# Kernel tuning notes

Measured on AMD Instinct MI355X. Metric: run time of the kernel, lower is better.

Reference implementation:

```python
import jax, jax.numpy as jnp
import numpy as np

T = 0.07          # temperature
K_POS = 5         # top-k positives per noun and for mask prediction
MARGIN = 0.1
LAM_CONTRAST = 0.6
LAM_MASK = 0.4


def _l2n(x):
    return x / jnp.linalg.norm(x, axis=-1, keepdims=True)


def setup_inputs() -> dict:
    key = jax.random.key(0)
    k0, k1, k2, k3 = jax.random.split(key, 4)
    B, N, D, M = 64, 576, 512, 16  # N = 24*24 patch grid
    patch_feats = _l2n(jax.random.normal(k0, (B, N, D), jnp.float32))
    noun_feats = _l2n(jax.random.normal(k1, (B, M, D), jnp.float32))
    global_img_feat = _l2n(jax.random.normal(k2, (B, D), jnp.float32))
    global_txt_feat = _l2n(jax.random.normal(k3, (B, D), jnp.float32))
    logit_scale = jnp.full((1,), 1.0 / 0.07, jnp.float32)
    idx = jnp.arange(B, dtype=jnp.int32)
    return {
        "patch_feats": patch_feats,
        "noun_feats": noun_feats,
        "global_img_feat": global_img_feat,
        "global_txt_feat": global_txt_feat,
        "logit_scale": logit_scale,
        "idx": idx,
    }


def _fine_grained_loss(patch_feats, noun_feats):
    # sim[b,m,n] = <noun_m, patch_n>; replaces the nested Python loops.
    B = patch_feats.shape[0]
    sim = jnp.einsum('bmd,bnd->bmn', noun_feats, patch_feats)
    scaled = sim / T
    # Per-noun contrastive loss. log_softmax over cat([topk, rest]) equals
    # log_softmax over all N entries evaluated at the topk positions, so:
    #   loss = -sum_topk log_softmax = K_POS*lse - sum(topk scaled values)
    lse = jax.nn.logsumexp(scaled, axis=-1)              # [B, M]
    topv, _ = jax.lax.top_k(scaled, K_POS)               # [B, M, K]
    contrast_loss = jnp.mean(K_POS * lse - topv.sum(-1))
    # Mask-prediction BCE loss (pool_type='mean').
    pooled = sim.mean(axis=1)                            # [B, N]
    _, tidx = jax.lax.top_k(pooled, K_POS)               # [B, K]
    pred = jnp.zeros_like(pooled).at[jnp.arange(B)[:, None], tidx].set(1.0)
    x = pooled / T
    mask_loss = jnp.mean(jnp.logaddexp(0.0, x) - x * pred)
    return LAM_CONTRAST * contrast_loss + LAM_MASK * mask_loss


def _contrastive_loss(img, txt, logit_scale, idx):
    logits = logit_scale.reshape(()) * (img @ txt.T)
    pos = (idx[:, None] == idx[None, :]).astype(logits.dtype)
    labels = pos / pos.sum(axis=1, keepdims=True)
    li2t = -(jax.nn.log_softmax(logits, axis=1) * labels).sum(1).mean()
    lt2i = -(jax.nn.log_softmax(logits.T, axis=1) * labels).sum(1).mean()
    return 0.5 * (li2t + lt2i)


def _triplet_loss(img, txt):
    scores = img @ txt.T
    d = jnp.diagonal(scores)
    eye = jnp.eye(scores.shape[0], dtype=bool)
    cost_s = jnp.where(eye, 0.0, jnp.clip(MARGIN + scores - d[:, None], 0.0)).sum()
    cost_im = jnp.where(eye, 0.0, jnp.clip(MARGIN + scores - d[None, :], 0.0)).sum()
    return 0.5 * (cost_s + cost_im)


def reference(patch_feats, noun_feats, global_img_feat, global_txt_feat, logit_scale, idx):
    loss_c = _contrastive_loss(global_img_feat, global_txt_feat, logit_scale, idx)
    loss_t = _triplet_loss(global_img_feat, global_txt_feat)
    loss_f = _fine_grained_loss(patch_feats, noun_feats)
    return jnp.stack([loss_c, loss_t, loss_f])
```

## Files before the change

kernel.cpp:

```cpp
#include <hip/hip_runtime.h>
#include <hip/hip_bf16.h>
#include <math.h>

#define NB 64
#define NN 576
#define ND 512
#define NM 16
#define QPB 9
#define KPOS 5
#define TINV 14.2857142857142857f

#define NFINE (NB * QPB)
#define NBLK1 (NFINE + NB)
#define WS_REC_OFF 4096
#define RECSZ 144
#define WS_NOUNF (WS_REC_OFF + NFINE * RECSZ)

#define FINF __builtin_inff()

typedef __attribute__((ext_vector_type(8))) short short8;
typedef __attribute__((ext_vector_type(4))) float floatx4;

__device__ __forceinline__ unsigned pk2(float lo, float hi) {
  return __builtin_amdgcn_perm(__float_as_uint(hi), __float_as_uint(lo), 0x07060302u);
}

__device__ __forceinline__ short8 packB(const float4 a, const float4 b) {
  union { unsigned u[4]; short8 s; } cv;
  cv.u[0] = pk2(a.x, a.y);
  cv.u[1] = pk2(a.z, a.w);
  cv.u[2] = pk2(b.x, b.y);
  cv.u[3] = pk2(b.z, b.w);
  return cv.s;
}

__device__ __forceinline__ void ins5(float (&a)[5], float v) {
  if (v > a[4]) {
    a[4] = v;
    if (a[4] > a[3]) { float x = a[4]; a[4] = a[3]; a[3] = x; }
    if (a[3] > a[2]) { float x = a[3]; a[3] = a[2]; a[2] = x; }
    if (a[2] > a[1]) { float x = a[2]; a[2] = a[1]; a[1] = x; }
    if (a[1] > a[0]) { float x = a[1]; a[1] = a[0]; a[0] = x; }
  }
}

__device__ __forceinline__ void merge5(float (&a)[5], const float (&b)[5]) {
  float r[5];
#pragma unroll
  for (int k = 0; k < 5; ++k) {
    float best = -FINF;
#pragma unroll
    for (int i = 0; i <= k + 1; ++i) {
      const int j = k + 1 - i;
      const float av = (i == 0) ? FINF : a[i - 1];
      const float bv = (j == 0) ? FINF : b[j - 1];
      best = fmaxf(best, fminf(av, bv));
    }
    r[k] = best;
  }
#pragma unroll
  for (int k = 0; k < 5; ++k) a[k] = r[k];
}

__device__ __forceinline__ void merge5_shfl(float (&a)[5], int msk) {
  float o[5];
#pragma unroll
  for (int k = 0; k < 5; ++k) o[k] = __shfl_xor(a[k], msk, 64);
  merge5(a, o);
}

__global__ __launch_bounds__(256) void k_prep(
    const float* __restrict__ noun, float* __restrict__ ws) {
  const int i = blockIdx.x * 256 + threadIdx.x;
  const float4 v = ((const float4*)noun)[i];
  unsigned ux = __float_as_uint(v.x), uy = __float_as_uint(v.y);
  unsigned uz = __float_as_uint(v.z), uw = __float_as_uint(v.w);
  ux += 0x7FFFu + ((ux >> 16) & 1u);
  uy += 0x7FFFu + ((uy >> 16) & 1u);
  uz += 0x7FFFu + ((uz >> 16) & 1u);
  uw += 0x7FFFu + ((uw >> 16) & 1u);
  uint2 o;
  o.x = __builtin_amdgcn_perm(uy, ux, 0x07060302u);
  o.y = __builtin_amdgcn_perm(uw, uz, 0x07060302u);
  ((uint2*)((unsigned short*)(ws + WS_NOUNF)))[i] = o;
}

__global__ __launch_bounds__(256) void k_sim(
    const float* __restrict__ patch, const float* __restrict__ gimg,
    const float* __restrict__ gtxt, float* __restrict__ ws) {
  const int blk = blockIdx.x;
  const int t = threadIdx.x;
  const int lane = t & 63;

  __shared__ float S[NM * 65];

  if (blk < NFINE) {
    const int b = blk / QPB, quad = blk - b * QPB;
    const int w = t >> 6;
    const int nidx = lane & 15;
    const int k0 = (lane >> 4) * 8;

    const unsigned short* nrow =
        (const unsigned short*)(ws + WS_NOUNF) + ((size_t)b * NM + nidx) * ND + k0;
    const float* prow =
        patch + ((size_t)(b * NN + quad * 64 + w * 16 + nidx)) * ND + k0;

    floatx4 acc = {0.f, 0.f, 0.f, 0.f};
#pragma unroll 4
    for (int ks = 0; ks < 16; ++ks) {
      const int o = ks * 32;
      const short8 af = *(const short8*)(nrow + o);
      const float4 p0 = *(const float4*)(prow + o);
      const float4 p1 = *(const float4*)(prow + o + 4);
      const short8 bf = packB(p0, p1);
      acc = __builtin_amdgcn_mfma_f32_16x16x32_bf16(af, bf, acc, 0, 0, 0);
    }

    const int mrow = (lane >> 4) * 4;
    const int pcol = w * 16 + nidx;
#pragma unroll
    for (int r = 0; r < 4; ++r) S[(mrow + r) * 65 + pcol] = acc[r] * TINV;
    __syncthreads();

    float* rec = ws + WS_REC_OFF + (size_t)blk * RECSZ;
    if (w == 1) {
      float x = 0.f;
#pragma unroll
      for (int m = 0; m < NM; ++m) x += S[m * 65 + lane];
      x *= (1.f / 16.f);
      float sxp = (x > 0.f) ? (x + log1pf(expf(-x))) : log1pf(expf(x));
      float t5[5] = {x, -FINF, -FINF, -FINF, -FINF};
#pragma unroll
      for (int msk = 1; msk < 64; msk <<= 1) {
        sxp += __shfl_xor(sxp, msk, 64);
        merge5_shfl(t5, msk);
      }
      if (lane == 0) {
        rec[128] = sxp;
#pragma unroll
        for (int k = 0; k < 5; ++k) rec[129 + k] = t5[k];
      }
    } else if (w == 0) {
      const int r_ = lane & 15;
      const int h = lane >> 4;
      const float* row = &S[r_ * 65 + h * 16];
      float mx = -FINF;
#pragma unroll
      for (int k = 0; k < 16; ++k) mx = fmaxf(mx, row[k]);
      mx = fmaxf(mx, __shfl_xor(mx, 16, 64));
      mx = fmaxf(mx, __shfl_xor(mx, 32, 64));
      float se = 0.f;
      float r5[5] = {-FINF, -FINF, -FINF, -FINF, -FINF};
#pragma unroll
      for (int k = 0; k < 16; ++k) {
        const float v = row[k];
        se += expf(v - mx);
        ins5(r5, v);
      }
      se += __shfl_xor(se, 16, 64);
      se += __shfl_xor(se, 32, 64);
      merge5_shfl(r5, 16);
      merge5_shfl(r5, 32);
      if (h == 0) {
        float* rr = rec + r_ * 8;
        rr[0] = mx;
        rr[1] = se;
#pragma unroll
        for (int k = 0; k < 5; ++k) rr[2 + k] = r5[k];
      }
    }
  } else {
    const int i = blk - NFINE;
    const int dq = t >> 6;
    const float4* ip = (const float4*)(gimg + (size_t)i * ND + dq * 128);
    const float4* tp = (const float4*)(gtxt + (size_t)lane * ND + dq * 128);
    float a = 0.f;
#pragma unroll
    for (int q = 0; q < 32; ++q) {
      const float4 x = ip[q];
      const float4 y = tp[q];
      a += x.x * y.x + x.y * y.y + x.z * y.z + x.w * y.w;
    }
    S[dq * 64 + lane] = a;
    __syncthreads();
    if (t < 64) ws[i * 64 + t] = S[t] + S[64 + t] + S[128 + t] + S[192 + t];
  }
}

__global__ __launch_bounds__(64) void k_final(
    const float* __restrict__ ws, const float* __restrict__ lscale,
    const int* __restrict__ idx, float* __restrict__ out) {
  const int blk = blockIdx.x;
  const int t = threadIdx.x;

  if (blk < NB) {
    const float* base = ws + WS_REC_OFF + (size_t)blk * QPB * RECSZ;
    const int m = t & 15;
    const int g = t >> 4;
    const int nq = (g == 0) ? 3 : 2;

    float lm[3], ls[3];
    float t5[5] = {-FINF, -FINF, -FINF, -FINF, -FINF};
#pragma unroll
    for (int i = 0; i < 3; ++i) { lm[i] = -FINF; ls[i] = 0.f; }
    float mx = -FINF;
    for (int i = 0; i < nq; ++i) {
      const float* rr = base + (g + 4 * i) * RECSZ + m * 8;
      lm[i] = rr[0]; ls[i] = rr[1];
      mx = fmaxf(mx, rr[0]);
#pragma unroll
      for (int k = 0; k < 5; ++k) ins5(t5, rr[2 + k]);
    }
    mx = fmaxf(mx, __shfl_xor(mx, 16, 64));
    mx = fmaxf(mx, __shfl_xor(mx, 32, 64));
    float S = 0.f;
    for (int i = 0; i < nq; ++i) S += ls[i] * expf(lm[i] - mx);
    S += __shfl_xor(S, 16, 64);
    S += __shfl_xor(S, 32, 64);
    merge5_shfl(t5, 16);
    merge5_shfl(t5, 32);

    float contrib = 0.f;
    if (g == 0) {
      const float lse = mx + logf(S);
      const float st = t5[0] + t5[1] + t5[2] + t5[3] + t5[4];
      contrib = (KPOS * lse - st) * (0.6f / (float)(NB * NM));
    }

    float sp_ = 0.f;
    float u5[5] = {-FINF, -FINF, -FINF, -FINF, -FINF};
    if (m == 0) {
      for (int i = 0; i < nq; ++i) {
        const float* rr = base + (g + 4 * i) * RECSZ + 128;
        sp_ += rr[0];
#pragma unroll
        for (int k = 0; k < 5; ++k) ins5(u5, rr[1 + k]);
      }
    }
    sp_ += __shfl_xor(sp_, 16, 64);
    sp_ += __shfl_xor(sp_, 32, 64);
    merge5_shfl(u5, 16);
    merge5_shfl(u5, 32);
    if (t == 0) {
      const float st = u5[0] + u5[1] + u5[2] + u5[3] + u5[4];
      contrib += (sp_ - st) * (0.4f / (float)(NB * NN));
    }
#pragma unroll
    for (int msk = 1; msk < 64; msk <<= 1) contrib += __shfl_xor(contrib, msk, 64);
    if (t == 0) atomicAdd(out + 2, contrib);
    return;
  }

  __shared__ float s[64 * 65];
  __shared__ float dg[64];
  __shared__ int idl[64];
  for (int i = 0; i < 64; ++i) s[i * 65 + t] = ws[i * 64 + t];
  idl[t] = idx[t];
  __syncthreads();
  dg[t] = s[t * 66];
  __syncthreads();
  const float sc = lscale[0];

  float mR = -FINF, mC = -FINF;
  for (int j = 0; j < 64; ++j) {
    mR = fmaxf(mR, sc * s[t * 65 + j]);
    mC = fmaxf(mC, sc * s[j * 65 + t]);
  }
  float seR = 0.f, seC = 0.f;
  for (int j = 0; j < 64; ++j) {
    seR += expf(sc * s[t * 65 + j] - mR);
    seC += expf(sc * s[j * 65 + t] - mC);
  }
  const float lseR = mR + logf(seR);
  const float lseC = mC + logf(seC);

  const int myid = idl[t];
  const float di = dg[t];
  float ps = 0.f, trow = 0.f, tcol = 0.f, cs = 0.f, ci = 0.f;
  for (int j = 0; j < 64; ++j) {
    const float sv = s[t * 65 + j];
    const float svT = s[j * 65 + t];
    if (idl[j] == myid) {
      ps += 1.f;
      trow += sc * sv - lseR;
      tcol += sc * svT - lseC;
    }
    if (j != t) {
      cs += fmaxf(0.f, 0.1f + sv - di);
      ci += fmaxf(0.f, 0.1f + sv - dg[j]);
    }
  }
  float vc = -(trow + tcol) / ps;
  float vt = cs + ci;
#pragma unroll
  for (int msk = 1; msk < 64; msk <<= 1) {
    vc += __shfl_xor(vc, msk, 64);
    vt += __shfl_xor(vt, msk, 64);
  }
  if (t == 0) {
    out[0] = vc * (0.5f / 64.f);
    out[1] = vt * 0.5f;
  }
}

extern "C" void kernel_launch(void* const* d_in, const int* in_sizes, int n_in,
                              void* d_out, int out_size, void* d_ws, size_t ws_size,
                              hipStream_t stream) {
  const float* patch = (const float*)d_in[0];
  const float* noun  = (const float*)d_in[1];
  const float* gimg  = (const float*)d_in[2];
  const float* gtxt  = (const float*)d_in[3];
  const float* lsc   = (const float*)d_in[4];
  const int*   idx   = (const int*)d_in[5];
  float* out = (float*)d_out;
  float* ws  = (float*)d_ws;

  hipMemsetAsync(d_out, 0, 3 * sizeof(float), stream);
  k_prep<<<dim3(512), dim3(256), 0, stream>>>(noun, ws);
  k_sim<<<dim3(NBLK1), dim3(256), 0, stream>>>(patch, gimg, gtxt, ws);
  k_final<<<dim3(NB + 1), dim3(64), 0, stream>>>(ws, lsc, idx, out);
}
```

Before: 136.1 us.

## Fuse final reduction into sim kernel via last-block-done atomic counter

Removes the separate k_final launch. Each k_sim block increments a global counter after a threadfence, and the last block to finish does the fine-grained loss aggregation and the global contrastive/triplet losses. This saves one kernel launch and its gap, and replaces the memset of the output with a memset of the counter. The cost is that all the final work now runs serially in one block instead of being spread over 65 blocks, which adds tail latency.

```diff
diff --git a/kernel.cpp b/kernel.cpp
--- a/kernel.cpp
+++ b/kernel.cpp
@@ -15,6 +15,7 @@
 #define WS_REC_OFF 4096
 #define RECSZ 144
 #define WS_NOUNF (WS_REC_OFF + NFINE * RECSZ)
+#define CNT_IDX (WS_NOUNF + 262144)
 
 #define FINF __builtin_inff()
 
@@ -87,16 +88,19 @@
 
 __global__ __launch_bounds__(256) void k_sim(
     const float* __restrict__ patch, const float* __restrict__ gimg,
-    const float* __restrict__ gtxt, float* __restrict__ ws) {
+    const float* __restrict__ gtxt, const float* __restrict__ lscale,
+    const int* __restrict__ idx, float* __restrict__ ws,
+    float* __restrict__ out) {
   const int blk = blockIdx.x;
   const int t = threadIdx.x;
   const int lane = t & 63;
-
-  __shared__ float S[NM * 65];
+  const int w = t >> 6;
+
+  __shared__ float S[4288];
+  __shared__ unsigned int winflag;
 
   if (blk < NFINE) {
     const int b = blk / QPB, quad = blk - b * QPB;
-    const int w = t >> 6;
     const int nidx = lane & 15;
     const int k0 = (lane >> 4) * 8;
 
@@ -171,9 +175,8 @@
     }
   } else {
     const int i = blk - NFINE;
-    const int dq = t >> 6;
-    const float4* ip = (const float4*)(gimg + (size_t)i * ND + dq * 128);
-    const float4* tp = (const float4*)(gtxt + (size_t)lane * ND + dq * 128);
+    const float4* ip = (const float4*)(gimg + (size_t)i * ND + w * 128);
+    const float4* tp = (const float4*)(gtxt + (size_t)lane * ND + w * 128);
     float a = 0.f;
 #pragma unroll
     for (int q = 0; q < 32; ++q) {
@@ -181,125 +184,109 @@
       const float4 y = tp[q];
       a += x.x * y.x + x.y * y.y + x.z * y.z + x.w * y.w;
     }
-    S[dq * 64 + lane] = a;
+    S[w * 64 + lane] = a;
     __syncthreads();
     if (t < 64) ws[i * 64 + t] = S[t] + S[64 + t] + S[128 + t] + S[192 + t];
   }
-}
-
-__global__ __launch_bounds__(64) void k_final(
-    const float* __restrict__ ws, const float* __restrict__ lscale,
-    const int* __restrict__ idx, float* __restrict__ out) {
-  const int blk = blockIdx.x;
-  const int t = threadIdx.x;
-
-  if (blk < NB) {
-    const float* base = ws + WS_REC_OFF + (size_t)blk * QPB * RECSZ;
-    const int m = t & 15;
-    const int g = t >> 4;
-    const int nq = (g == 0) ? 3 : 2;
-
-    float lm[3], ls[3];
+
+  __syncthreads();
+  __threadfence();
+  if (t == 0) {
+    const unsigned old = atomicAdd((unsigned int*)(ws + CNT_IDX), 1u);
+    winflag = (old == NBLK1 - 1) ? 1u : 0u;
+  }
+  __syncthreads();
+  if (!winflag) return;
+  __threadfence();
+
+  const float* recs = ws + WS_REC_OFF;
+  float local = 0.f;
+  for (int i = t; i < NB * NM; i += 256) {
+    const int b = i >> 4, m = i & 15;
+    const float* base = recs + (size_t)b * QPB * RECSZ + m * 8;
+    float mx = -FINF;
+#pragma unroll
+    for (int q = 0; q < QPB; ++q) mx = fmaxf(mx, base[q * RECSZ]);
+    float S5 = 0.f;
     float t5[5] = {-FINF, -FINF, -FINF, -FINF, -FINF};
 #pragma unroll
-    for (int i = 0; i < 3; ++i) { lm[i] = -FINF; ls[i] = 0.f; }
-    float mx = -FINF;
-    for (int i = 0; i < nq; ++i) {
-      const float* rr = base + (g + 4 * i) * RECSZ + m * 8;
-      lm[i] = rr[0]; ls[i] = rr[1];
-      mx = fmaxf(mx, rr[0]);
-#pragma unroll
-      for (int k = 0; k < 5; ++k) ins5(t5, rr[2 + k]);
-    }
-    mx = fmaxf(mx, __shfl_xor(mx, 16, 64));
-    mx = fmaxf(mx, __shfl_xor(mx, 32, 64));
-    float S = 0.f;
-    for (int i = 0; i < nq; ++i) S += ls[i] * expf(lm[i] - mx);
-    S += __shfl_xor(S, 16, 64);
-    S += __shfl_xor(S, 32, 64);
-    merge5_shfl(t5, 16);
-    merge5_shfl(t5, 32);
-
-    float contrib = 0.f;
-    if (g == 0) {
-      const float lse = mx + logf(S);
-      const float st = t5[0] + t5[1] + t5[2] + t5[3] + t5[4];
-      contrib = (KPOS * lse - st) * (0.6f / (float)(NB * NM));
-    }
-
-    float sp_ = 0.f;
+    for (int q = 0; q < QPB; ++q) {
+      S5 += base[q * RECSZ + 1] * expf(base[q * RECSZ] - mx);
+#pragma unroll
+      for (int k = 0; k < 5; ++k) ins5(t5, base[q * RECSZ + 2 + k]);
+    }
+    const float st = t5[0] + t5[1] + t5[2] + t5[3] + t5[4];
+    local += (KPOS * (mx + logf(S5)) - st) * (0.6f / (float)(NB * NM));
+  }
+  if (t < NB) {
+    const float* base = recs + (size_t)t * QPB * RECSZ + 128;
+    float sp = 0.f;
     float u5[5] = {-FINF, -FINF, -FINF, -FINF, -FINF};
-    if (m == 0) {
-      for (int i = 0; i < nq; ++i) {
-        const float* rr = base + (g + 4 * i) * RECSZ + 128;
-        sp_ += rr[0];
-#pragma unroll
-        for (int k = 0; k < 5; ++k) ins5(u5, rr[1 + k]);
-      }
-    }
-    sp_ += __shfl_xor(sp_, 16, 64);
-    sp_ += __shfl_xor(sp_, 32, 64);
-    merge5_shfl(u5, 16);
-    merge5_shfl(u5, 32);
+#pragma unroll
+    for (int q = 0; q < QPB; ++q) {
+      sp += base[q * RECSZ];
+#pragma unroll
+      for (int k = 0; k < 5; ++k) ins5(u5, base[q * RECSZ + 1 + k]);
+    }
+    const float st = u5[0] + u5[1] + u5[2] + u5[3] + u5[4];
+    local += (sp - st) * (0.4f / (float)(NB * NN));
+  }
+#pragma unroll
+  for (int msk = 1; msk < 64; msk <<= 1) local += __shfl_xor(local, msk, 64);
+  __syncthreads();
+  if (lane == 0) S[w] = local;
+  __syncthreads();
+  if (t == 0) out[2] = S[0] + S[1] + S[2] + S[3];
+  __syncthreads();
+
+  float* S_ = &S[0];
+  for (int i = t; i < 4096; i += 256) S_[(i >> 6) * 65 + (i & 63)] = ws[i];
+  __syncthreads();
+  float* dgp = &S[4160];
+  int* idl = (int*)&S[4224];
+  if (t < 64) { dgp[t] = S_[t * 66]; idl[t] = idx[t]; }
+  __syncthreads();
+  if (t < 64) {
+    const float sc = lscale[0];
+    float mR = -FINF, mC = -FINF;
+    for (int j = 0; j < 64; ++j) {
+      mR = fmaxf(mR, sc * S_[t * 65 + j]);
+      mC = fmaxf(mC, sc * S_[j * 65 + t]);
+    }
+    float seR = 0.f, seC = 0.f;
+    for (int j = 0; j < 64; ++j) {
+      seR += expf(sc * S_[t * 65 + j] - mR);
+      seC += expf(sc * S_[j * 65 + t] - mC);
+    }
+    const float lseR = mR + logf(seR);
+    const float lseC = mC + logf(seC);
+    const int myid = idl[t];
+    const float di = dgp[t];
+    float ps = 0.f, trow = 0.f, tcol = 0.f, cs = 0.f, ci = 0.f;
+    for (int j = 0; j < 64; ++j) {
+      const float sv = S_[t * 65 + j];
+      const float svT = S_[j * 65 + t];
+      if (idl[j] == myid) {
+        ps += 1.f;
+        trow += sc * sv - lseR;
+        tcol += sc * svT - lseC;
+      }
+      if (j != t) {
+        cs += fmaxf(0.f, 0.1f + sv - di);
+        ci += fmaxf(0.f, 0.1f + sv - dgp[j]);
+      }
+    }
+    float vc = -(trow + tcol) / ps;
+    float vt = cs + ci;
+#pragma unroll
+    for (int msk = 1; msk < 64; msk <<= 1) {
+      vc += __shfl_xor(vc, msk, 64);
+      vt += __shfl_xor(vt, msk, 64);
+    }
     if (t == 0) {
-      const float st = u5[0] + u5[1] + u5[2] + u5[3] + u5[4];
-      contrib += (sp_ - st) * (0.4f / (float)(NB * NN));
-    }
-#pragma unroll
-    for (int msk = 1; msk < 64; msk <<= 1) contrib += __shfl_xor(contrib, msk, 64);
-    if (t == 0) atomicAdd(out + 2, contrib);
-    return;
-  }
-
-  __shared__ float s[64 * 65];
-  __shared__ float dg[64];
-  __shared__ int idl[64];
-  for (int i = 0; i < 64; ++i) s[i * 65 + t] = ws[i * 64 + t];
-  idl[t] = idx[t];
-  __syncthreads();
-  dg[t] = s[t * 66];
-  __syncthreads();
-  const float sc = lscale[0];
-
-  float mR = -FINF, mC = -FINF;
-  for (int j = 0; j < 64; ++j) {
-    mR = fmaxf(mR, sc * s[t * 65 + j]);
-    mC = fmaxf(mC, sc * s[j * 65 + t]);
-  }
-  float seR = 0.f, seC = 0.f;
-  for (int j = 0; j < 64; ++j) {
-    seR += expf(sc * s[t * 65 + j] - mR);
-    seC += expf(sc * s[j * 65 + t] - mC);
-  }
-  const float lseR = mR + logf(seR);
-  const float lseC = mC + logf(seC);
-
-  const int myid = idl[t];
-  const float di = dg[t];
-  float ps = 0.f, trow = 0.f, tcol = 0.f, cs = 0.f, ci = 0.f;
-  for (int j = 0; j < 64; ++j) {
-    const float sv = s[t * 65 + j];
-    const float svT = s[j * 65 + t];
-    if (idl[j] == myid) {
-      ps += 1.f;
-      trow += sc * sv - lseR;
-      tcol += sc * svT - lseC;
-    }
-    if (j != t) {
-      cs += fmaxf(0.f, 0.1f + sv - di);
-      ci += fmaxf(0.f, 0.1f + sv - dg[j]);
-    }
-  }
-  float vc = -(trow + tcol) / ps;
-  float vt = cs + ci;
-#pragma unroll
-  for (int msk = 1; msk < 64; msk <<= 1) {
-    vc += __shfl_xor(vc, msk, 64);
-    vt += __shfl_xor(vt, msk, 64);
-  }
-  if (t == 0) {
-    out[0] = vc * (0.5f / 64.f);
-    out[1] = vt * 0.5f;
+      out[0] = vc * (0.5f / 64.f);
+      out[1] = vt * 0.5f;
+    }
   }
 }
 
@@ -315,8 +302,7 @@
   float* out = (float*)d_out;
   float* ws  = (float*)d_ws;
 
-  hipMemsetAsync(d_out, 0, 3 * sizeof(float), stream);
+  hipMemsetAsync((char*)d_ws + (size_t)CNT_IDX * sizeof(float), 0, 4, stream);
   k_prep<<<dim3(512), dim3(256), 0, stream>>>(noun, ws);
-  k_sim<<<dim3(NBLK1), dim3(256), 0, stream>>>(patch, gimg, gtxt, ws);
-  k_final<<<dim3(NB + 1), dim3(64), 0, stream>>>(ws, lsc, idx, out);
-}
+  k_sim<<<dim3(NBLK1), dim3(256), 0, stream>>>(patch, gimg, gtxt, lsc, idx, ws, out);
+}
```

Result: slower. 244.0 us (+79.3%).
